# Kernel tuning notes

Hardware: AMD Instinct MI355X
Metric: run time of the kernel (lower is better)

## Reference

```python
import jax, jax.numpy as jnp
import numpy as np

NWIN = 128
HOP = NWIN // 2
BUCKET_FREQS = (32, 32, 64, 64, 64)   # partition of the 256 f-bins (ragged_shapes[-3])
BUCKET_TIMES = (16, 32, 48, 64, 128)  # per-bucket nb_m_bins (ragged_shapes[-1])
EPS = 1e-5


def _bn_relu(x, gamma, beta, axes):
    """Training-mode BatchNorm over `axes` (channel axis = 1) + ReLU, fused."""
    mean = jnp.mean(x, axis=axes, keepdims=True)
    var = jnp.var(x, axis=axes, keepdims=True)  # biased var, as torch BN uses
    bshape = (1, x.shape[1]) + (1,) * (x.ndim - 2)
    g = gamma.reshape(bshape)
    b = beta.reshape(bshape)
    return jax.nn.relu((x - mean) * jax.lax.rsqrt(var + EPS) * g + b)


def setup_inputs() -> dict:
    key = jax.random.key(0)
    ks = jax.random.split(key, 24)
    B, C, F, S = 8, 2, 256, 64
    ncoefs = (S + 1) * HOP  # 4160
    inp = {
        "x": jax.random.normal(ks[0], (B, C, F, ncoefs), jnp.float32),
        "input_mean": jax.random.normal(ks[1], (F,), jnp.float32),
        "input_scale": jax.random.uniform(ks[2], (F,), jnp.float32, 0.5, 1.5),
        "W_deo": jax.random.normal(ks[3], (NWIN, 2 * NWIN), jnp.float32) / np.sqrt(2 * NWIN),
        "gamma_deo": jax.random.uniform(ks[4], (C,), jnp.float32, 0.5, 1.5),
        "beta_deo": 0.1 * jax.random.normal(ks[5], (C,), jnp.float32),
        "nb_slices": S,
    }
    for i, mt in enumerate(BUCKET_TIMES):
        inp[f"W_di{i}"] = jax.random.normal(ks[6 + i], (mt, NWIN), jnp.float32) / np.sqrt(NWIN)
        inp[f"g_di{i}"] = jax.random.uniform(ks[11 + i], (C,), jnp.float32, 0.5, 1.5)
        inp[f"b_di{i}"] = 0.1 * jax.random.normal(ks[16 + i], (C,), jnp.float32)
    return inp


def reference(x, input_mean, input_scale, W_deo, gamma_deo, beta_deo,
              W_di0, W_di1, W_di2, W_di3, W_di4,
              g_di0, g_di1, g_di2, g_di3, g_di4,
              b_di0, b_di1, b_di2, b_di3, b_di4,
              nb_slices):
    # input normalization (permute/add/mul/permute == broadcast over f-bins)
    x = (x + input_mean[:, None]) * input_scale[:, None]  # [B,C,F,T]

    # ---- deoverlap_add: all overlapping windows at once ----
    # torch loop reads slicq[ptr-hop : ptr+nwin+hop] with left pad (slice 0)
    # and right pad (last slice); equivalently pad both ends by HOP and take
    # windows of length 2*NWIN starting at i*HOP.
    x_pad = jnp.pad(x, ((0, 0), (0, 0), (0, 0), (HOP, HOP)))
    win_idx = (jnp.arange(nb_slices)[:, None] * HOP
               + jnp.arange(2 * NWIN)[None, :])          # [S, 2W]
    windows = x_pad[..., win_idx]                        # [B,C,F,S,2W]
    y = jnp.einsum('bcfsw,nw->bcfsn', windows, W_deo)    # [B,C,F,S,W]
    # original applies BN per slice call -> batch stats per (channel, slice)
    y = _bn_relu(y, gamma_deo, beta_deo, axes=(0, 2, 4))

    # ---- deinterpolate: ragged per-bucket Linear + BN3d + ReLU ----
    W_di = (W_di0, W_di1, W_di2, W_di3, W_di4)
    g_di = (g_di0, g_di1, g_di2, g_di3, g_di4)
    b_di = (b_di0, b_di1, b_di2, b_di3, b_di4)
    outs = []
    p = 0
    for freqs, W, g, b in zip(BUCKET_FREQS, W_di, g_di, b_di):
        z = jnp.einsum('bcfst,mt->bcfsm', y[:, :, p:p + freqs], W)
        outs.append(_bn_relu(z, g, b, axes=(0, 2, 3, 4)))
        p += freqs
    return tuple(outs)
```

## Files before the change

### kernel.cpp

```cpp
#include <hip/hip_runtime.h>
#include <hip/hip_bf16.h>
#include <cstddef>

#define BB   8
#define CC   2
#define FF   256
#define TT   4160
#define SS   64
#define NW   128
#define KW   256
#define EPSV 1e-5f

typedef __attribute__((ext_vector_type(8))) short bf16x8;
typedef __attribute__((ext_vector_type(4))) float f32x4;
typedef __attribute__((ext_vector_type(4))) unsigned int u32x4;

#define YOFF    0
#define ZOFF    16777216
#define W1OFF   25427968
#define W2OFF   25444352
#define STATF   25462784
#define OFF_DA     256
#define OFF_DB     384
#define OFF_DIAB   544
#define OFF_STATR  1024
#define OFF_STATR2 17408
#define STAT_NZ 19456

__device__ __forceinline__ unsigned short f2bf(float f) {
    unsigned int u = __builtin_bit_cast(unsigned int, f);
    u = (u + 0x7FFFu + ((u >> 16) & 1u)) >> 16;
    return (unsigned short)u;
}
__device__ __forceinline__ float bf2f(unsigned short h) {
    return __builtin_bit_cast(float, (unsigned int)h << 16);
}
__device__ __forceinline__ unsigned int pk2bf(float lo, float hi) {
    float2 f; f.x = lo; f.y = hi;
    __hip_bfloat162 h = __float22bfloat162_rn(f);
    unsigned int r;
    __builtin_memcpy(&r, &h, 4);
    return r;
}

__global__ __launch_bounds__(256) void k_prep(
    const float* __restrict__ Wdeo,
    const float* __restrict__ Wdi0, const float* __restrict__ Wdi1,
    const float* __restrict__ Wdi2, const float* __restrict__ Wdi3,
    const float* __restrict__ Wdi4,
    unsigned short* __restrict__ w1, unsigned short* __restrict__ w2,
    float* __restrict__ statz)
{
    int gid = blockIdx.x * 256 + threadIdx.x;
    if (gid < STAT_NZ) statz[gid] = 0.f;
    int id = gid - STAT_NZ;
    if (id >= 0 && id < 32768) {
        int j = id & 7, lane = (id >> 3) & 63, nt = (id >> 9) & 7, ks = id >> 12;
        int n = nt * 16 + (lane & 15);
        int k = ks * 32 + ((lane >> 4) << 3) + j;
        w1[id] = f2bf(Wdeo[n * KW + k]);
    }
    id -= 32768;
    if (id >= 0 && id < 36864) {
        const float* W; int base, Tk;
        if (id < 2048)       { W = Wdi0; base = 0;     Tk = 1; }
        else if (id < 6144)  { W = Wdi1; base = 2048;  Tk = 2; }
        else if (id < 12288) { W = Wdi2; base = 6144;  Tk = 3; }
        else if (id < 20480) { W = Wdi3; base = 12288; Tk = 4; }
        else                 { W = Wdi4; base = 20480; Tk = 8; }
        int e = id - base;
        int j = e & 7, lane = (e >> 3) & 63, rest = e >> 9;
        int t = rest % Tk, ks = rest / Tk;
        int n = t * 16 + (lane & 15);
        int k = ks * 32 + ((lane >> 4) << 3) + j;
        w2[id] = f2bf(W[n * NW + k]);
    }
}

__global__ __launch_bounds__(256) void k_deoverlap(
    const float* __restrict__ x, const float* __restrict__ imean,
    const float* __restrict__ iscale, const unsigned short* __restrict__ w1,
    unsigned short* __restrict__ y, float* __restrict__ statR)
{
    __shared__ __align__(16) unsigned short xs[4288];
    __shared__ float psA[4][64], pqA[4][64];
    const int tid = threadIdx.x;
    const int r   = blockIdx.x;
    const int c   = (r >> 8) & 1;
    const int lane = tid & 63, wv = tid >> 6;
    const int q = lane >> 4, m = lane & 15;

    bf16x8 Bc0 = *(const bf16x8*)(w1 + ((size_t)((2 * wv + 0) * 64 + lane) << 3));
    bf16x8 Bc1 = *(const bf16x8*)(w1 + ((size_t)((2 * wv + 1) * 64 + lane) << 3));
    bf16x8 Bn0 = *(const bf16x8*)(w1 + ((size_t)((8 + 2 * wv + 0) * 64 + lane) << 3));
    bf16x8 Bn1 = *(const bf16x8*)(w1 + ((size_t)((8 + 2 * wv + 1) * 64 + lane) << 3));

    {
        const float mval = imean[r & 255], sval = iscale[r & 255];
        const float* xr = x + (size_t)r * TT;
        float4 xv[5];
#pragma unroll
        for (int k = 0; k < 5; ++k) {
            int p4 = tid + k * 256;
            float4 v; v.x = 0.f; v.y = 0.f; v.z = 0.f; v.w = 0.f;
            if (p4 >= 16 && p4 < 1056)
                v = *(const float4*)&xr[p4 * 4 - 64];
            xv[k] = v;
        }
#pragma unroll
        for (int k = 0; k < 5; ++k) {
            int p4 = tid + k * 256;
            if (p4 < 1072) {
                int i = p4 * 4;
                int phys = i ^ (((i >> 6) & 7) << 3);
                uint2 pk;
                if (p4 >= 16 && p4 < 1056) {
                    pk.x = pk2bf((xv[k].x + mval) * sval, (xv[k].y + mval) * sval);
                    pk.y = pk2bf((xv[k].z + mval) * sval, (xv[k].w + mval) * sval);
                } else {
                    pk.x = 0u; pk.y = 0u;
                }
                *(uint2*)&xs[phys] = pk;
            }
        }
    }
    __syncthreads();

    f32x4 acc[4][2] = {};
#pragma unroll
    for (int ks = 0; ks < 8; ++ks) {
        bf16x8 Bm0, Bm1;
        if (ks < 6) {
            Bm0 = *(const bf16x8*)(w1 + ((size_t)(((ks + 2) * 8 + 2 * wv + 0) * 64 + lane) << 3));
            Bm1 = *(const bf16x8*)(w1 + ((size_t)(((ks + 2) * 8 + 2 * wv + 1) * 64 + lane) << 3));
        }
        const int k0 = ks * 32;
#pragma unroll
        for (int st = 0; st < 4; ++st) {
            int idx  = (st * 16 + m) * 64 + k0 + q * 8;
            int phys = idx ^ (((idx >> 6) & 7) << 3);
            bf16x8 A = *(const bf16x8*)&xs[phys];
            acc[st][0] = __builtin_amdgcn_mfma_f32_16x16x32_bf16(Bc0, A, acc[st][0], 0, 0, 0);
            acc[st][1] = __builtin_amdgcn_mfma_f32_16x16x32_bf16(Bc1, A, acc[st][1], 0, 0, 0);
        }
        Bc0 = Bn0; Bc1 = Bn1;
        Bn0 = Bm0; Bn1 = Bm1;
    }

#pragma unroll
    for (int st = 0; st < 4; ++st) {
        float ps = 0.f, pq = 0.f;
#pragma unroll
        for (int t = 0; t < 2; ++t) {
            uint2 u;
            u.x = pk2bf(acc[st][t][0], acc[st][t][1]);
            u.y = pk2bf(acc[st][t][2], acc[st][t][3]);
            *(uint2*)&y[(size_t)r * 8192 + (st * 16 + m) * NW + (2 * wv + t) * 16 + q * 4] = u;
#pragma unroll
            for (int reg = 0; reg < 4; ++reg) {
                float v = acc[st][t][reg];
                ps += v; pq += v * v;
            }
        }
        ps += __shfl_xor(ps, 16, 64);  pq += __shfl_xor(pq, 16, 64);
        ps += __shfl_xor(ps, 32, 64);  pq += __shfl_xor(pq, 32, 64);
        if (q == 0) { psA[wv][st * 16 + m] = ps; pqA[wv][st * 16 + m] = pq; }
    }
    __syncthreads();
    if (tid < 128) {
        int s = tid & 63, which = tid >> 6;
        float v = which ? (pqA[0][s] + pqA[1][s] + pqA[2][s] + pqA[3][s])
                        : (psA[0][s] + psA[1][s] + psA[2][s] + psA[3][s]);
        int rep = blockIdx.x & 63;
        atomicAdd(&statR[rep * 256 + which * 128 + c * SS + s], v);
    }
}

__global__ void k_deo_ab(const float* __restrict__ statR,
                         const float* __restrict__ g, const float* __restrict__ be,
                         float* __restrict__ da, float* __restrict__ db)
{
    __shared__ float red[4][256];
    int tid = threadIdx.x;
    int i = tid & 127, h = tid >> 7;
    float sm = 0.f, sq = 0.f;
    for (int rep = h; rep < 64; rep += 4) {
        sm += statR[rep * 256 + i];
        sq += statR[rep * 256 + 128 + i];
    }
    red[h][i] = sm; red[h][128 + i] = sq;
    __syncthreads();
    if (h == 0) {
        sm = red[0][i] + red[1][i] + red[2][i] + red[3][i];
        sq = red[0][128 + i] + red[1][128 + i] + red[2][128 + i] + red[3][128 + i];
        int c = i >> 6;
        const float N = (float)(BB * FF * NW);
        float mean = sm / N;
        float var  = sq / N - mean * mean;
        float a = g[c] * rsqrtf(var + EPSV);
        da[i] = a;
        db[i] = be[c] - mean * a;
    }
}

template <int Tk, int G>
__device__ __forceinline__ void deinterp_body(
    int sub,
    const unsigned short* __restrict__ y, const unsigned short* __restrict__ wb,
    const float* __restrict__ da, const float* __restrict__ db,
    unsigned short* __restrict__ zz, float* __restrict__ statR2,
    int p, int freqs, int kidx, float* ssum, float* ssq)
{
    constexpr int MT = Tk * 16;
    const int tid = threadIdx.x, lane = tid & 63, wv = tid >> 6;
    const int q = lane >> 4, m = lane & 15;
    const int bc = sub & 15;
    const int fg = sub >> 4;
    const int c  = bc & 1;
    const int s  = wv * 16 + m;
    const float aS = da[c * SS + s], bS = db[c * SS + s];

    f32x4 acc[G][Tk] = {};
    const unsigned short* ybase = y + ((size_t)(bc * FF + p + fg * G) * SS) * NW;

#pragma unroll
    for (int ks = 0; ks < 4; ++ks) {
        bf16x8 B[Tk];
#pragma unroll
        for (int t = 0; t < Tk; ++t)
            B[t] = *(const bf16x8*)(wb + ((size_t)((ks * Tk + t) * 64 + lane) << 3));
#pragma unroll
        for (int g = 0; g < G; ++g) {
            bf16x8 ar = *(const bf16x8*)(ybase + ((size_t)g * SS + s) * NW + ks * 32 + q * 8);
            u32x4 tp;
#pragma unroll
            for (int jj = 0; jj < 4; ++jj) {
                float f0 = fmaxf(fmaf(bf2f((unsigned short)ar[2 * jj]),     aS, bS), 0.f);
                float f1 = fmaxf(fmaf(bf2f((unsigned short)ar[2 * jj + 1]), aS, bS), 0.f);
                tp[jj] = pk2bf(f0, f1);
            }
            bf16x8 af;
            __builtin_memcpy(&af, &tp, 16);
#pragma unroll
            for (int t = 0; t < Tk; ++t)
                acc[g][t] = __builtin_amdgcn_mfma_f32_16x16x32_bf16(B[t], af, acc[g][t], 0, 0, 0);
        }
    }

    float ls = 0.f, lq = 0.f;
#pragma unroll
    for (int g = 0; g < G; ++g) {
        size_t zrow = ((size_t)(bc * freqs + fg * G + g) * SS + wv * 16 + m) * MT;
#pragma unroll
        for (int t = 0; t < Tk; ++t) {
            uint2 u;
            u.x = pk2bf(acc[g][t][0], acc[g][t][1]);
            u.y = pk2bf(acc[g][t][2], acc[g][t][3]);
            *(uint2*)&zz[zrow + t * 16 + q * 4] = u;
#pragma unroll
            for (int reg = 0; reg < 4; ++reg) {
                float v = acc[g][t][reg];
                ls += v; lq += v * v;
            }
        }
    }
#pragma unroll
    for (int o = 32; o > 0; o >>= 1) {
        ls += __shfl_down(ls, o, 64);
        lq += __shfl_down(lq, o, 64);
    }
    if (lane == 0) { ssum[wv] = ls; ssq[wv] = lq; }
    __syncthreads();
    if (tid == 0) {
        int rep = sub & 63;
        atomicAdd(&statR2[rep * 32 + kidx * 2 + c],      ssum[0] + ssum[1] + ssum[2] + ssum[3]);
        atomicAdd(&statR2[rep * 32 + 16 + kidx * 2 + c], ssq[0] + ssq[1] + ssq[2] + ssq[3]);
    }
}

__global__ __launch_bounds__(256) void k_deinterp_all(
    const unsigned short* __restrict__ y, const unsigned short* __restrict__ w2,
    const float* __restrict__ da, const float* __restrict__ db,
    unsigned short* __restrict__ z, float* __restrict__ statR2)
{
    __shared__ float ssum[4], ssq[4];
    const int b = blockIdx.x;
    if (b < 512) {
        deinterp_body<4, 2>(b,        y, w2 + 12288, da, db, z + 4718592, statR2, 128, 64, 3, ssum, ssq);
    } else if (b < 1024) {
        deinterp_body<3, 2>(b - 512,  y, w2 + 6144,  da, db, z + 1572864, statR2,  64, 64, 2, ssum, ssq);
    } else if (b < 2048) {
        deinterp_body<8, 1>(b - 1024, y, w2 + 20480, da, db, z + 8912896, statR2, 192, 64, 4, ssum, ssq);
    } else if (b < 2304) {
        deinterp_body<2, 2>(b - 2048, y, w2 + 2048,  da, db, z + 524288,  statR2,  32, 32, 1, ssum, ssq);
    } else {
        deinterp_body<1, 2>(b - 2304, y, w2 + 0,     da, db, z + 0,       statR2,   0, 32, 0, ssum, ssq);
    }
}

__global__ void k_di_ab(const float* __restrict__ statR2,
                        const float* __restrict__ g0, const float* __restrict__ g1,
                        const float* __restrict__ g2, const float* __restrict__ g3,
                        const float* __restrict__ g4,
                        const float* __restrict__ b0, const float* __restrict__ b1,
                        const float* __restrict__ b2, const float* __restrict__ b3,
                        const float* __restrict__ b4,
                        float* __restrict__ ab)
{
    int tid = threadIdx.x;
    int i = tid >> 4, j = tid & 15;
    if (i < 10) {
        float sm = 0.f, sq = 0.f;
        for (int rep = j; rep < 64; rep += 16) {
            sm += statR2[rep * 32 + i];
            sq += statR2[rep * 32 + 16 + i];
        }
#pragma unroll
        for (int o = 8; o > 0; o >>= 1) {
            sm += __shfl_down(sm, o, 16);
            sq += __shfl_down(sq, o, 16);
        }
        if (j == 0) {
            int kb = i >> 1, c = i & 1;
            const float Nv[5] = {262144.f, 524288.f, 1572864.f, 2097152.f, 4194304.f};
            const float* gp[5] = {g0, g1, g2, g3, g4};
            const float* bp[5] = {b0, b1, b2, b3, b4};
            float mean = sm / Nv[kb];
            float var  = sq / Nv[kb] - mean * mean;
            float a = gp[kb][c] * rsqrtf(var + EPSV);
            ab[i * 2]     = a;
            ab[i * 2 + 1] = bp[kb][c] - mean * a;
        }
    }
}

__device__ __forceinline__ void bn_class(int i4, const float* __restrict__ ab,
                                         float& a, float& b)
{
    int kb, off4, cs4;
    if (i4 < 131072)       { kb = 0; off4 = 0;       cs4 = 8192;   }
    else if (i4 < 393216)  { kb = 1; off4 = 131072;  cs4 = 16384;  }
    else if (i4 < 1179648) { kb = 2; off4 = 393216;  cs4 = 49152;  }
    else if (i4 < 2228224) { kb = 3; off4 = 1179648; cs4 = 65536;  }
    else                   { kb = 4; off4 = 2228224; cs4 = 131072; }
    int c = ((i4 - off4) / cs4) & 1;
    a = ab[(kb * 2 + c) * 2];
    b = ab[(kb * 2 + c) * 2 + 1];
}

__global__ __launch_bounds__(256) void k_bn_out(
    const unsigned short* __restrict__ z, const float* __restrict__ ab,
    float* __restrict__ out)
{
    int i4a = blockIdx.x * 512 + threadIdx.x;
    int i4b = i4a + 256;

    ushort4 ua = *(const ushort4*)(z + (size_t)i4a * 4);
    ushort4 ub = *(const ushort4*)(z + (size_t)i4b * 4);

    float aA, bA, aB, bB;
    bn_class(i4a, ab, aA, bA);
    bn_class(i4b, ab, aB, bB);

    float4 oa, ob;
    oa.x = fmaxf(fmaf(bf2f(ua.x), aA, bA), 0.f);
    oa.y = fmaxf(fmaf(bf2f(ua.y), aA, bA), 0.f);
    oa.z = fmaxf(fmaf(bf2f(ua.z), aA, bA), 0.f);
    oa.w = fmaxf(fmaf(bf2f(ua.w), aA, bA), 0.f);
    ob.x = fmaxf(fmaf(bf2f(ub.x), aB, bB), 0.f);
    ob.y = fmaxf(fmaf(bf2f(ub.y), aB, bB), 0.f);
    ob.z = fmaxf(fmaf(bf2f(ub.z), aB, bB), 0.f);
    ob.w = fmaxf(fmaf(bf2f(ub.w), aB, bB), 0.f);

    *(float4*)(out + (size_t)i4a * 4) = oa;
    *(float4*)(out + (size_t)i4b * 4) = ob;
}

extern "C" void kernel_launch(void* const* d_in, const int* in_sizes, int n_in,
                              void* d_out, int out_size, void* d_ws, size_t ws_size,
                              hipStream_t stream)
{
    const float* x      = (const float*)d_in[0];
    const float* imean  = (const float*)d_in[1];
    const float* iscale = (const float*)d_in[2];
    const float* Wdeo   = (const float*)d_in[3];
    const float* gdeo   = (const float*)d_in[4];
    const float* bdeo   = (const float*)d_in[5];
    const float* Wdi[5] = {(const float*)d_in[7],  (const float*)d_in[10],
                           (const float*)d_in[13], (const float*)d_in[16],
                           (const float*)d_in[19]};
    const float* gdi[5] = {(const float*)d_in[8],  (const float*)d_in[11],
                           (const float*)d_in[14], (const float*)d_in[17],
                           (const float*)d_in[20]};
    const float* bdi[5] = {(const float*)d_in[9],  (const float*)d_in[12],
                           (const float*)d_in[15], (const float*)d_in[18],
                           (const float*)d_in[21]};
    float* out = (float*)d_out;
    float* ws  = (float*)d_ws;

    unsigned short* y  = (unsigned short*)(ws + YOFF);
    unsigned short* z  = (unsigned short*)(ws + ZOFF);
    unsigned short* w1 = (unsigned short*)(ws + W1OFF);
    unsigned short* w2 = (unsigned short*)(ws + W2OFF);
    float* st     = ws + STATF;
    float* da     = st + OFF_DA;
    float* db     = st + OFF_DB;
    float* diab   = st + OFF_DIAB;
    float* statR  = st + OFF_STATR;
    float* statR2 = st + OFF_STATR2;

    k_prep<<<348, 256, 0, stream>>>(Wdeo, Wdi[0], Wdi[1], Wdi[2], Wdi[3], Wdi[4],
                                    w1, w2, st);

    k_deoverlap<<<BB * CC * FF, 256, 0, stream>>>(x, imean, iscale, w1, y, statR);
    k_deo_ab<<<1, 512, 0, stream>>>(statR, gdeo, bdeo, da, db);

    k_deinterp_all<<<2560, 256, 0, stream>>>(y, w2, da, db, z, statR2);

    k_di_ab<<<1, 160, 0, stream>>>(statR2,
                                   gdi[0], gdi[1], gdi[2], gdi[3], gdi[4],
                                   bdi[0], bdi[1], bdi[2], bdi[3], bdi[4], diab);

    k_bn_out<<<8448, 256, 0, stream>>>(z, diab, out);
}
```

Before: 230.8 us.

## Process four rows per deoverlap block with double-buffered LDS prefetch

Each k_deoverlap block now handles four consecutive (b,c,f) rows instead of one. The next row's global loads are issued before the current row's MFMA work, and the converted row goes into a second LDS buffer, so load latency overlaps compute. BN statistics are accumulated in registers across rows and reduced once, which cuts the atomics per row by a factor of four. The trade-offs are a quarter as many blocks, twice the LDS, more register pressure from holding the prefetched rows, and reloading the weight fragments for every row.

```diff
diff --git a/kernel.cpp b/kernel.cpp
--- a/kernel.cpp
+++ b/kernel.cpp
@@ -10,6 +10,7 @@
 #define NW   128
 #define KW   256
 #define EPSV 1e-5f
+#define RPB  4
 
 typedef __attribute__((ext_vector_type(8))) short bf16x8;
 typedef __attribute__((ext_vector_type(4))) float f32x4;
@@ -77,91 +78,117 @@
     }
 }
 
+__device__ __forceinline__ void deo_load_row(const float* __restrict__ xr, int tid,
+                                             float4* xv)
+{
+#pragma unroll
+    for (int k = 0; k < 5; ++k) {
+        int p4 = tid + k * 256;
+        float4 v; v.x = 0.f; v.y = 0.f; v.z = 0.f; v.w = 0.f;
+        if (p4 >= 16 && p4 < 1056)
+            v = *(const float4*)&xr[p4 * 4 - 64];
+        xv[k] = v;
+    }
+}
+__device__ __forceinline__ void deo_write_row(unsigned short* __restrict__ xsb, int tid,
+                                              const float4* xv, float mval, float sval)
+{
+#pragma unroll
+    for (int k = 0; k < 5; ++k) {
+        int p4 = tid + k * 256;
+        if (p4 < 1072) {
+            int i = p4 * 4;
+            int phys = i ^ (((i >> 6) & 7) << 3);
+            uint2 pk;
+            if (p4 >= 16 && p4 < 1056) {
+                pk.x = pk2bf((xv[k].x + mval) * sval, (xv[k].y + mval) * sval);
+                pk.y = pk2bf((xv[k].z + mval) * sval, (xv[k].w + mval) * sval);
+            } else {
+                pk.x = 0u; pk.y = 0u;
+            }
+            *(uint2*)&xsb[phys] = pk;
+        }
+    }
+}
+
 __global__ __launch_bounds__(256) void k_deoverlap(
     const float* __restrict__ x, const float* __restrict__ imean,
     const float* __restrict__ iscale, const unsigned short* __restrict__ w1,
     unsigned short* __restrict__ y, float* __restrict__ statR)
 {
-    __shared__ __align__(16) unsigned short xs[4288];
+    __shared__ __align__(16) unsigned short xs[2][4288];
     __shared__ float psA[4][64], pqA[4][64];
     const int tid = threadIdx.x;
-    const int r   = blockIdx.x;
-    const int c   = (r >> 8) & 1;
+    const int r0  = blockIdx.x * RPB;
+    const int c   = (r0 >> 8) & 1;
     const int lane = tid & 63, wv = tid >> 6;
     const int q = lane >> 4, m = lane & 15;
 
-    bf16x8 Bc0 = *(const bf16x8*)(w1 + ((size_t)((2 * wv + 0) * 64 + lane) << 3));
-    bf16x8 Bc1 = *(const bf16x8*)(w1 + ((size_t)((2 * wv + 1) * 64 + lane) << 3));
-    bf16x8 Bn0 = *(const bf16x8*)(w1 + ((size_t)((8 + 2 * wv + 0) * 64 + lane) << 3));
-    bf16x8 Bn1 = *(const bf16x8*)(w1 + ((size_t)((8 + 2 * wv + 1) * 64 + lane) << 3));
-
-    {
-        const float mval = imean[r & 255], sval = iscale[r & 255];
-        const float* xr = x + (size_t)r * TT;
-        float4 xv[5];
-#pragma unroll
-        for (int k = 0; k < 5; ++k) {
-            int p4 = tid + k * 256;
-            float4 v; v.x = 0.f; v.y = 0.f; v.z = 0.f; v.w = 0.f;
-            if (p4 >= 16 && p4 < 1056)
-                v = *(const float4*)&xr[p4 * 4 - 64];
-            xv[k] = v;
-        }
-#pragma unroll
-        for (int k = 0; k < 5; ++k) {
-            int p4 = tid + k * 256;
-            if (p4 < 1072) {
-                int i = p4 * 4;
-                int phys = i ^ (((i >> 6) & 7) << 3);
-                uint2 pk;
-                if (p4 >= 16 && p4 < 1056) {
-                    pk.x = pk2bf((xv[k].x + mval) * sval, (xv[k].y + mval) * sval);
-                    pk.y = pk2bf((xv[k].z + mval) * sval, (xv[k].w + mval) * sval);
-                } else {
-                    pk.x = 0u; pk.y = 0u;
+    float statS[4] = {0.f, 0.f, 0.f, 0.f};
+    float statQ[4] = {0.f, 0.f, 0.f, 0.f};
+
+    float4 xv[5];
+    deo_load_row(x + (size_t)r0 * TT, tid, xv);
+    deo_write_row(xs[0], tid, xv, imean[r0 & 255], iscale[r0 & 255]);
+    __syncthreads();
+
+#pragma unroll
+    for (int rr = 0; rr < RPB; ++rr) {
+        const int r = r0 + rr;
+        float mnext = 0.f, snext = 0.f;
+        if (rr < RPB - 1) {
+            deo_load_row(x + (size_t)(r + 1) * TT, tid, xv);
+            mnext = imean[(r0 & 255) + rr + 1];
+            snext = iscale[(r0 & 255) + rr + 1];
+        }
+
+        const unsigned short* xsb = xs[rr & 1];
+        f32x4 acc[4][2] = {};
+        bf16x8 Bc0 = *(const bf16x8*)(w1 + ((size_t)((2 * wv + 0) * 64 + lane) << 3));
+        bf16x8 Bc1 = *(const bf16x8*)(w1 + ((size_t)((2 * wv + 1) * 64 + lane) << 3));
+#pragma unroll
+        for (int ks = 0; ks < 8; ++ks) {
+            bf16x8 Bn0, Bn1;
+            if (ks < 7) {
+                Bn0 = *(const bf16x8*)(w1 + ((size_t)(((ks + 1) * 8 + 2 * wv + 0) * 64 + lane) << 3));
+                Bn1 = *(const bf16x8*)(w1 + ((size_t)(((ks + 1) * 8 + 2 * wv + 1) * 64 + lane) << 3));
+            }
+            const int k0 = ks * 32;
+#pragma unroll
+            for (int st = 0; st < 4; ++st) {
+                int idx  = (st * 16 + m) * 64 + k0 + q * 8;
+                int phys = idx ^ (((idx >> 6) & 7) << 3);
+                bf16x8 A = *(const bf16x8*)&xsb[phys];
+                acc[st][0] = __builtin_amdgcn_mfma_f32_16x16x32_bf16(Bc0, A, acc[st][0], 0, 0, 0);
+                acc[st][1] = __builtin_amdgcn_mfma_f32_16x16x32_bf16(Bc1, A, acc[st][1], 0, 0, 0);
+            }
+            Bc0 = Bn0; Bc1 = Bn1;
+        }
+
+#pragma unroll
+        for (int st = 0; st < 4; ++st)
+#pragma unroll
+            for (int t = 0; t < 2; ++t) {
+                uint2 u;
+                u.x = pk2bf(acc[st][t][0], acc[st][t][1]);
+                u.y = pk2bf(acc[st][t][2], acc[st][t][3]);
+                *(uint2*)&y[(size_t)r * 8192 + (st * 16 + m) * NW + (2 * wv + t) * 16 + q * 4] = u;
+#pragma unroll
+                for (int reg = 0; reg < 4; ++reg) {
+                    float v = acc[st][t][reg];
+                    statS[st] += v; statQ[st] += v * v;
                 }
-                *(uint2*)&xs[phys] = pk;
-            }
-        }
-    }
-    __syncthreads();
-
-    f32x4 acc[4][2] = {};
-#pragma unroll
-    for (int ks = 0; ks < 8; ++ks) {
-        bf16x8 Bm0, Bm1;
-        if (ks < 6) {
-            Bm0 = *(const bf16x8*)(w1 + ((size_t)(((ks + 2) * 8 + 2 * wv + 0) * 64 + lane) << 3));
-            Bm1 = *(const bf16x8*)(w1 + ((size_t)(((ks + 2) * 8 + 2 * wv + 1) * 64 + lane) << 3));
-        }
-        const int k0 = ks * 32;
-#pragma unroll
-        for (int st = 0; st < 4; ++st) {
-            int idx  = (st * 16 + m) * 64 + k0 + q * 8;
-            int phys = idx ^ (((idx >> 6) & 7) << 3);
-            bf16x8 A = *(const bf16x8*)&xs[phys];
-            acc[st][0] = __builtin_amdgcn_mfma_f32_16x16x32_bf16(Bc0, A, acc[st][0], 0, 0, 0);
-            acc[st][1] = __builtin_amdgcn_mfma_f32_16x16x32_bf16(Bc1, A, acc[st][1], 0, 0, 0);
-        }
-        Bc0 = Bn0; Bc1 = Bn1;
-        Bn0 = Bm0; Bn1 = Bm1;
+            }
+
+        if (rr < RPB - 1) {
+            deo_write_row(xs[(rr + 1) & 1], tid, xv, mnext, snext);
+            __syncthreads();
+        }
     }
 
 #pragma unroll
     for (int st = 0; st < 4; ++st) {
-        float ps = 0.f, pq = 0.f;
-#pragma unroll
-        for (int t = 0; t < 2; ++t) {
-            uint2 u;
-            u.x = pk2bf(acc[st][t][0], acc[st][t][1]);
-            u.y = pk2bf(acc[st][t][2], acc[st][t][3]);
-            *(uint2*)&y[(size_t)r * 8192 + (st * 16 + m) * NW + (2 * wv + t) * 16 + q * 4] = u;
-#pragma unroll
-            for (int reg = 0; reg < 4; ++reg) {
-                float v = acc[st][t][reg];
-                ps += v; pq += v * v;
-            }
-        }
+        float ps = statS[st], pq = statQ[st];
         ps += __shfl_xor(ps, 16, 64);  pq += __shfl_xor(pq, 16, 64);
         ps += __shfl_xor(ps, 32, 64);  pq += __shfl_xor(pq, 32, 64);
         if (q == 0) { psA[wv][st * 16 + m] = ps; pqA[wv][st * 16 + m] = pq; }
@@ -412,7 +439,7 @@
     k_prep<<<348, 256, 0, stream>>>(Wdeo, Wdi[0], Wdi[1], Wdi[2], Wdi[3], Wdi[4],
                                     w1, w2, st);
 
-    k_deoverlap<<<BB * CC * FF, 256, 0, stream>>>(x, imean, iscale, w1, y, statR);
+    k_deoverlap<<<(BB * CC * FF) / RPB, 256, 0, stream>>>(x, imean, iscale, w1, y, statR);
     k_deo_ab<<<1, 512, 0, stream>>>(statR, gdeo, bdeo, da, db);
 
     k_deinterp_all<<<2560, 256, 0, stream>>>(y, w2, da, db, z, statR2);
```

Measured after the change: 231.6 us. Within noise of the previous version (+0.4%).
